# Kernel tuning notes

Hardware: AMD Instinct MI355X
Metric: run time of the kernel (lower is better)

The kernel has to match this reference:

```python
import jax, jax.numpy as jnp
import numpy as np
from jax import lax

B, T, D_IN, D_OUT = 1, 24000, 598, 3
UNITS = [100, 100, 100]
EPS = 0.001


def _lstm(x, W, U, b):
    # x: [B,T,D]; W: [D,4U]; U: [U,4U]; b: [4U]. Keras gate order i,f,g,o.
    units = U.shape[0]
    xW = jnp.einsum('btd,dk->btk', x, W) + b  # precompute input projections

    def step(carry, xw_t):
        h, c = carry
        z = xw_t + h @ U
        i, f, g, o = jnp.split(z, 4, axis=-1)
        c = jax.nn.sigmoid(f) * c + jax.nn.sigmoid(i) * jnp.tanh(g)
        h = jax.nn.sigmoid(o) * jnp.tanh(c)
        return (h, c), h

    h0 = jnp.zeros((x.shape[0], units), x.dtype)
    (_, _), hs = lax.scan(step, (h0, h0), jnp.swapaxes(xW, 0, 1))
    return jnp.swapaxes(hs, 0, 1)  # [B,T,U]


def _bn(x, gamma, beta, mean, var):
    # inference-mode batch norm over last axis
    return (x - mean) * lax.rsqrt(var + EPS) * gamma + beta


def setup_inputs() -> dict:
    key = jax.random.key(0)
    ks = jax.random.split(key, 16)
    out = {"x": jax.random.normal(ks[0], (B, T, D_IN), jnp.float32)}
    d_prev = D_IN
    ki = 1
    for l, u in enumerate(UNITS, start=1):
        out[f"W{l}"] = jax.random.normal(ks[ki], (d_prev, 4 * u), jnp.float32) * (2.0 / d_prev) ** 0.5; ki += 1
        out[f"U{l}"] = jax.random.normal(ks[ki], (u, 4 * u), jnp.float32) * (1.0 / u) ** 0.5; ki += 1
        out[f"b{l}"] = jnp.zeros((4 * u,), jnp.float32)
        out[f"g{l}"] = jnp.ones((u,), jnp.float32)
        out[f"be{l}"] = jnp.zeros((u,), jnp.float32)
        out[f"m{l}"] = jnp.zeros((u,), jnp.float32)
        out[f"v{l}"] = jnp.ones((u,), jnp.float32)
        d_prev = u
    out["Wd"] = jax.random.normal(ks[ki], (d_prev, D_OUT), jnp.float32) * (2.0 / d_prev) ** 0.5
    out["bd"] = jnp.zeros((D_OUT,), jnp.float32)
    return out


def reference(x, W1, U1, b1, g1, be1, m1, v1,
              W2, U2, b2, g2, be2, m2, v2,
              W3, U3, b3, g3, be3, m3, v3, Wd, bd):
    h = x
    params = [(W1, U1, b1, g1, be1, m1, v1),
              (W2, U2, b2, g2, be2, m2, v2),
              (W3, U3, b3, g3, be3, m3, v3)]
    for (W, U, b, g, be, m, v) in params:
        h = _lstm(h, W, U, b)
        h = _bn(h, g, be, m, v)
    return jax.nn.softmax(h @ Wd + bd, axis=-1)
```

## Files before the change

### kernel.cpp

```cpp
#include <hip/hip_runtime.h>

#define T_STEPS 24000
#define DIN 598
#define NU 100
#define NG 400
#define KHALF 52
#define KPAD 104
#define CHUNK 240
#define NCHUNK 100
#define RING 4
#define RN (RING * CHUNK)

#define BARRIER_LDS() asm volatile("s_waitcnt lgkmcnt(0)\n\ts_barrier" ::: "memory")

__device__ __forceinline__ void wg_wait_ge(int* flag, int target) {
    if (threadIdx.x == 0) {
        while (__hip_atomic_load(flag, __ATOMIC_RELAXED, __HIP_MEMORY_SCOPE_AGENT) < target)
            __builtin_amdgcn_s_sleep(2);
    }
    __syncthreads();
    __builtin_amdgcn_fence(__ATOMIC_ACQUIRE, "agent");
}
__device__ __forceinline__ void wg_publish(int* a, int va, int* b, int vb) {
    __syncthreads();
    if (threadIdx.x == 0) {
        if (a) __hip_atomic_store(a, va, __ATOMIC_RELEASE, __HIP_MEMORY_SCOPE_AGENT);
        if (b) __hip_atomic_store(b, vb, __ATOMIC_RELEASE, __HIP_MEMORY_SCOPE_AGENT);
    }
}

__device__ __forceinline__ float sigmoid_(float x) {
    return 1.f / (1.f + __expf(-x));
}
__device__ __forceinline__ float tanh_(float x) {
    float e = __expf(2.f * x);
    return 1.f - 2.f / (e + 1.f);
}

__global__ __launch_bounds__(256) void gemm_bias_kernel(
    const float* __restrict__ A, const float* __restrict__ B,
    const float* __restrict__ bias, float* __restrict__ C,
    int M, int N, int K)
{
    __shared__ float As[16][65];
    __shared__ float Bs[16][65];
    const int tid = threadIdx.x;
    const int tx = tid & 15;
    const int ty = tid >> 4;
    const int bm = blockIdx.y * 64;
    const int bn = blockIdx.x * 64;
    float acc[4][4] = {};

    for (int k0 = 0; k0 < K; k0 += 16) {
        #pragma unroll
        for (int p = 0; p < 4; ++p) {
            int e = tid + p * 256;
            int r = e >> 4, cc = e & 15;
            int m = bm + r, k = k0 + cc;
            float v = (m < M && k < K) ? A[(long)m * K + k] : 0.f;
            As[cc][r] = v;
        }
        #pragma unroll
        for (int p = 0; p < 4; ++p) {
            int e = tid + p * 256;
            int r = e >> 6, cc = e & 63;
            int k = k0 + r, n = bn + cc;
            float v = (k < K && n < N) ? B[(long)k * N + n] : 0.f;
            Bs[r][cc] = v;
        }
        __syncthreads();
        #pragma unroll
        for (int kk = 0; kk < 16; ++kk) {
            float a[4], b[4];
            #pragma unroll
            for (int i = 0; i < 4; ++i) a[i] = As[kk][ty * 4 + i];
            #pragma unroll
            for (int j = 0; j < 4; ++j) b[j] = Bs[kk][tx * 4 + j];
            #pragma unroll
            for (int i = 0; i < 4; ++i)
                #pragma unroll
                for (int j = 0; j < 4; ++j)
                    acc[i][j] += a[i] * b[j];
        }
        __syncthreads();
    }
    #pragma unroll
    for (int i = 0; i < 4; ++i) {
        int m = bm + ty * 4 + i;
        if (m >= M) continue;
        #pragma unroll
        for (int j = 0; j < 4; ++j) {
            int n = bn + tx * 4 + j;
            if (n < N) {
                int pn = (n % 100) * 4 + (n / 100);
                C[(long)m * N + pn] = acc[i][j] + bias[n];
            }
        }
    }
}

__device__ void rec_role(
    const float* __restrict__ xz, int xz_ring,
    const float* __restrict__ U,
    float* __restrict__ hout, long h_stride, int h_ring,
    int* flag_up, int* done_self, int* done_down, int* flag_self,
    float* lds)
{
    float* hb0 = lds;
    float* hb1 = lds + KPAD;
    const int tid = threadIdx.x;
    const bool active = tid < 2 * NU;
    const int u = tid >> 1;
    const int s = tid & 1;

    float4 uf[KHALF];
    if (active) {
        const int k0 = KHALF * s;
        #pragma unroll
        for (int i = 0; i < KHALF; ++i) {
            int k = k0 + i;
            uf[i] = (k < NU)
                ? make_float4(U[(long)k * NG + u],       U[(long)k * NG + NU + u],
                              U[(long)k * NG + 2 * NU + u], U[(long)k * NG + 3 * NU + u])
                : make_float4(0.f, 0.f, 0.f, 0.f);
        }
    }
    if (tid < KPAD) { hb0[tid] = 0.f; hb1[tid] = 0.f; }
    float c_state = 0.f;
    float2 xw0 = make_float2(0.f, 0.f), xw1 = xw0;
    float4 hbatch = make_float4(0.f, 0.f, 0.f, 0.f);
    __syncthreads();

    auto step = [&](const float* hrd, float* hwr, int t) {
        if (active) {
            const float4* h4 = (const float4*)(hrd + KHALF * s);
            float ax = 0.f, ay = 0.f, az = 0.f, aw = 0.f;
            #pragma unroll
            for (int q = 0; q < 13; ++q) {
                float4 hv = h4[q];
                float hh[4] = {hv.x, hv.y, hv.z, hv.w};
                #pragma unroll
                for (int j = 0; j < 4; ++j) {
                    float4 uv = uf[4 * q + j];
                    ax += uv.x * hh[j];
                    ay += uv.y * hh[j];
                    az += uv.z * hh[j];
                    aw += uv.w * hh[j];
                }
            }
            if (s == 0) { ax += xw0.x; ay += xw0.y; }
            else        { az += xw0.x; aw += xw0.y; }
            xw0 = xw1;
            int tp = t + 2;
            if (tp < T_STEPS) {
                long rr = xz_ring ? (long)(tp % RN) : (long)tp;
                xw1 = *(const float2*)&xz[rr * NG + 4 * u + 2 * s];
            }
            ax += __shfl_xor(ax, 1);
            ay += __shfl_xor(ay, 1);
            az += __shfl_xor(az, 1);
            aw += __shfl_xor(aw, 1);
            float iv = sigmoid_(ax);
            float fv = sigmoid_(ay);
            float gv = tanh_(az);
            float ov = sigmoid_(aw);
            c_state = fv * c_state + iv * gv;
            float h = ov * tanh_(c_state);
            if (s == 0) {
                hwr[u] = h;
                int ph = t & 3;
                if      (ph == 0) hbatch.x = h;
                else if (ph == 1) hbatch.y = h;
                else if (ph == 2) hbatch.z = h;
                else {
                    hbatch.w = h;
                    long tb = h_ring ? (long)((t - 3) % RN) : (long)(t - 3);
                    *(float4*)&hout[(long)u * h_stride + tb] = hbatch;
                }
            }
        }
        BARRIER_LDS();
    };

    for (int c = 0; c < NCHUNK; ++c) {
        if (flag_up) {
            int tgt = c + 2; if (tgt > NCHUNK) tgt = NCHUNK;
            wg_wait_ge(flag_up, tgt);
        }
        if (done_down && c >= RING) wg_wait_ge(done_down, c - RING + 1);
        if (c == 0 && active) {
            xw0 = *(const float2*)&xz[4 * u + 2 * s];
            xw1 = *(const float2*)&xz[NG + 4 * u + 2 * s];
        }
        const int t0 = c * CHUNK;
        for (int tt = 0; tt < CHUNK; tt += 2) {
            step(hb0, hb1, t0 + tt);
            step(hb1, hb0, t0 + tt + 1);
        }
        wg_publish(done_self, c + 1, flag_self, c + 1);
    }
}

__device__ void proj_role(
    const float* __restrict__ hin,
    const float* __restrict__ W,
    const float* __restrict__ bias,
    const float* __restrict__ g, const float* __restrict__ be,
    const float* __restrict__ m, const float* __restrict__ v,
    float* __restrict__ xzout,
    int* flag_up, int* done_self, int* done_down, int* flag_self,
    float* lds)
{
    const int tid = threadIdx.x;
    const bool active = tid < 2 * NU;
    const int u = tid >> 1;
    const int s = tid & 1;

    float4 wf[KHALF];
    float bx = 0.f, by = 0.f;
    if (active) {
        const int k0 = KHALF * s;
        float pbx = 0.f, pby = 0.f, pbz = 0.f, pbw = 0.f;
        #pragma unroll
        for (int i = 0; i < KHALF; ++i) {
            int k = k0 + i;
            if (k < NU) {
                float sc = g[k] * rsqrtf(v[k] + 1e-3f);
                float sh = be[k] - m[k] * sc;
                float w0 = W[(long)k * NG + u];
                float w1 = W[(long)k * NG + NU + u];
                float w2 = W[(long)k * NG + 2 * NU + u];
                float w3 = W[(long)k * NG + 3 * NU + u];
                wf[i] = make_float4(sc * w0, sc * w1, sc * w2, sc * w3);
                pbx += sh * w0; pby += sh * w1; pbz += sh * w2; pbw += sh * w3;
            } else {
                wf[i] = make_float4(0.f, 0.f, 0.f, 0.f);
            }
        }
        pbx += __shfl_xor(pbx, 1); pby += __shfl_xor(pby, 1);
        pbz += __shfl_xor(pbz, 1); pbw += __shfl_xor(pbw, 1);
        if (s == 0) { bx = bias[u]          + pbx; by = bias[NU + u]     + pby; }
        else        { bx = bias[2 * NU + u] + pbz; by = bias[3 * NU + u] + pbw; }
    }

    for (int c = 0; c < NCHUNK; ++c) {
        wg_wait_ge(flag_up, c + 1);
        if (c >= RING) wg_wait_ge(done_down, c - RING + 1);
        {
            const int tbase = (c % RING) * CHUNK;
            for (int idx = tid; idx < KPAD * CHUNK; idx += 256) {
                int k = idx / CHUNK, r = idx - k * CHUNK;
                lds[r * KPAD + k] = (k < NU) ? hin[(long)k * RN + tbase + r] : 0.f;
            }
        }
        wg_publish(done_self, c + 1, (int*)0, 0);
        if (active) {
            float* ob = xzout + (size_t)(c % RING) * CHUNK * NG;
            for (int r = 0; r < CHUNK; ++r) {
                const float4* h4 = (const float4*)(lds + r * KPAD + KHALF * s);
                float ax = 0.f, ay = 0.f, az = 0.f, aw = 0.f;
                #pragma unroll
                for (int q = 0; q < 13; ++q) {
                    float4 hv = h4[q];
                    float hh[4] = {hv.x, hv.y, hv.z, hv.w};
                    #pragma unroll
                    for (int j = 0; j < 4; ++j) {
                        float4 wv = wf[4 * q + j];
                        ax += wv.x * hh[j];
                        ay += wv.y * hh[j];
                        az += wv.z * hh[j];
                        aw += wv.w * hh[j];
                    }
                }
                ax += __shfl_xor(ax, 1);
                ay += __shfl_xor(ay, 1);
                az += __shfl_xor(az, 1);
                aw += __shfl_xor(aw, 1);
                float2 o2 = (s == 0) ? make_float2(ax + bx, ay + by)
                                     : make_float2(az + bx, aw + by);
                *(float2*)&ob[(long)r * NG + 4 * u + 2 * s] = o2;
            }
        }
        wg_publish(flag_self, c + 1, (int*)0, 0);
    }
}

__global__ __launch_bounds__(256, 1) void lstm_pipe_kernel(
    const float* xw1, const float* U1,
    const float* U2, const float* W2, const float* b2,
    const float* U3, const float* W3, const float* b3,
    const float* g1, const float* be1, const float* m1, const float* v1,
    const float* g2, const float* be2, const float* m2, const float* v2,
    float* h1r, float* h2r, float* xz2r, float* xz3r, float* h3,
    int* f)
{
    extern __shared__ float smem[];
    int* f_h1  = f +   0;
    int* d_p2  = f +  32;
    int* f_xz2 = f +  64;
    int* d_r2  = f +  96;
    int* f_h2  = f + 128;
    int* d_p3  = f + 160;
    int* f_xz3 = f + 192;
    int* d_r3  = f + 224;

    switch (blockIdx.x) {
    case 0: rec_role(xw1, 0, U1, h1r, RN, 1, (int*)0, (int*)0, d_p2, f_h1, smem); break;
    case 1: proj_role(h1r, W2, b2, g1, be1, m1, v1, xz2r, f_h1, d_p2, d_r2, f_xz2, smem); break;
    case 2: rec_role(xz2r, 1, U2, h2r, RN, 1, f_xz2, d_r2, d_p3, f_h2, smem); break;
    case 3: proj_role(h2r, W3, b3, g2, be2, m2, v2, xz3r, f_h2, d_p3, d_r3, f_xz3, smem); break;
    case 4: rec_role(xz3r, 1, U3, h3, T_STEPS, 0, f_xz3, d_r3, (int*)0, (int*)0, smem); break;
    }
}

__global__ __launch_bounds__(256) void dense_softmax_kernel(
    const float* __restrict__ H,
    const float* __restrict__ Wd,
    const float* __restrict__ bd,
    const float* __restrict__ g3, const float* __restrict__ be3,
    const float* __restrict__ m3, const float* __restrict__ v3,
    float* __restrict__ out, int T)
{
    __shared__ float w[300];
    __shared__ float b[3];
    const int tid = threadIdx.x;
    for (int i = tid; i < 300; i += 256) {
        int k = i / 3;
        float sc = g3[k] * rsqrtf(v3[k] + 1e-3f);
        w[i] = Wd[i] * sc;
    }
    if (tid < 3) {
        float acc = bd[tid];
        for (int k = 0; k < NU; ++k) {
            float sc = g3[k] * rsqrtf(v3[k] + 1e-3f);
            float sh = be3[k] - m3[k] * sc;
            acc += sh * Wd[3 * k + tid];
        }
        b[tid] = acc;
    }
    __syncthreads();

    int row = blockIdx.x * blockDim.x + tid;
    if (row >= T) return;
    float s0 = b[0], s1 = b[1], s2 = b[2];
    #pragma unroll 4
    for (int k = 0; k < NU; ++k) {
        float hv = H[(long)k * T + row];
        s0 += hv * w[3 * k + 0];
        s1 += hv * w[3 * k + 1];
        s2 += hv * w[3 * k + 2];
    }
    float mx = fmaxf(s0, fmaxf(s1, s2));
    float e0 = __expf(s0 - mx), e1 = __expf(s1 - mx), e2 = __expf(s2 - mx);
    float inv = 1.f / (e0 + e1 + e2);
    out[(long)row * 3 + 0] = e0 * inv;
    out[(long)row * 3 + 1] = e1 * inv;
    out[(long)row * 3 + 2] = e2 * inv;
}

extern "C" void kernel_launch(void* const* d_in, const int* in_sizes, int n_in,
                              void* d_out, int out_size, void* d_ws, size_t ws_size,
                              hipStream_t stream)
{
    const float* x   = (const float*)d_in[0];
    const float* W1  = (const float*)d_in[1];
    const float* U1  = (const float*)d_in[2];
    const float* b1  = (const float*)d_in[3];
    const float* ga1 = (const float*)d_in[4];
    const float* be1 = (const float*)d_in[5];
    const float* mu1 = (const float*)d_in[6];
    const float* va1 = (const float*)d_in[7];
    const float* W2  = (const float*)d_in[8];
    const float* U2  = (const float*)d_in[9];
    const float* b2  = (const float*)d_in[10];
    const float* ga2 = (const float*)d_in[11];
    const float* be2 = (const float*)d_in[12];
    const float* mu2 = (const float*)d_in[13];
    const float* va2 = (const float*)d_in[14];
    const float* W3  = (const float*)d_in[15];
    const float* U3  = (const float*)d_in[16];
    const float* b3  = (const float*)d_in[17];
    const float* ga3 = (const float*)d_in[18];
    const float* be3 = (const float*)d_in[19];
    const float* mu3 = (const float*)d_in[20];
    const float* va3 = (const float*)d_in[21];
    const float* Wd  = (const float*)d_in[22];
    const float* bd  = (const float*)d_in[23];

    float* xw1  = (float*)d_ws;
    float* h3   = xw1  + (size_t)T_STEPS * NG;
    float* h1r  = h3   + (size_t)T_STEPS * NU;
    float* h2r  = h1r  + (size_t)RN * NU;
    float* xz2r = h2r  + (size_t)RN * NU;
    float* xz3r = xz2r + (size_t)RN * NG;
    int*   flags = (int*)(xz3r + (size_t)RN * NG);
    float* out = (float*)d_out;

    dim3 blk(256);
    dim3 grd((NG + 63) / 64, (T_STEPS + 63) / 64);

    gemm_bias_kernel<<<grd, blk, 0, stream>>>(x, W1, b1, xw1, T_STEPS, NG, DIN);
    hipMemsetAsync(flags, 0, 512 * sizeof(int), stream);
    lstm_pipe_kernel<<<5, 256, CHUNK * KPAD * sizeof(float), stream>>>(
        xw1, U1, U2, W2, b2, U3, W3, b3,
        ga1, be1, mu1, va1, ga2, be2, mu2, va2,
        h1r, h2r, xz2r, xz3r, h3, flags);
    dense_softmax_kernel<<<(T_STEPS + 255) / 256, 256, 0, stream>>>(
        h3, Wd, bd, ga3, be3, mu3, va3, out, T_STEPS);
}
```

Baseline: 18.85 ms.

## Split LSTM recurrence gates across 4 lanes per unit with 512-thread blocks

```diff
diff --git a/kernel.cpp b/kernel.cpp
--- a/kernel.cpp
+++ b/kernel.cpp
@@ -10,6 +10,7 @@
 #define NCHUNK 100
 #define RING 4
 #define RN (RING * CHUNK)
+#define BLK 512
 
 #define BARRIER_LDS() asm volatile("s_waitcnt lgkmcnt(0)\n\ts_barrier" ::: "memory")
 
@@ -109,20 +110,21 @@
     float* hb0 = lds;
     float* hb1 = lds + KPAD;
     const int tid = threadIdx.x;
-    const bool active = tid < 2 * NU;
-    const int u = tid >> 1;
-    const int s = tid & 1;
-
-    float4 uf[KHALF];
+    const bool active = tid < 4 * NU;
+    const int u  = tid >> 2;
+    const int gp = (tid >> 1) & 1;
+    const int s  = tid & 1;
+
+    float2 uf[KHALF];
     if (active) {
         const int k0 = KHALF * s;
         #pragma unroll
         for (int i = 0; i < KHALF; ++i) {
             int k = k0 + i;
             uf[i] = (k < NU)
-                ? make_float4(U[(long)k * NG + u],       U[(long)k * NG + NU + u],
-                              U[(long)k * NG + 2 * NU + u], U[(long)k * NG + 3 * NU + u])
-                : make_float4(0.f, 0.f, 0.f, 0.f);
+                ? make_float2(U[(long)k * NG + 2 * gp * NU + u],
+                              U[(long)k * NG + (2 * gp + 1) * NU + u])
+                : make_float2(0.f, 0.f);
         }
     }
     if (tid < KPAD) { hb0[tid] = 0.f; hb1[tid] = 0.f; }
@@ -134,39 +136,40 @@
     auto step = [&](const float* hrd, float* hwr, int t) {
         if (active) {
             const float4* h4 = (const float4*)(hrd + KHALF * s);
-            float ax = 0.f, ay = 0.f, az = 0.f, aw = 0.f;
+            float ax = 0.f, ay = 0.f;
             #pragma unroll
             for (int q = 0; q < 13; ++q) {
                 float4 hv = h4[q];
                 float hh[4] = {hv.x, hv.y, hv.z, hv.w};
                 #pragma unroll
                 for (int j = 0; j < 4; ++j) {
-                    float4 uv = uf[4 * q + j];
+                    float2 uv = uf[4 * q + j];
                     ax += uv.x * hh[j];
                     ay += uv.y * hh[j];
-                    az += uv.z * hh[j];
-                    aw += uv.w * hh[j];
                 }
             }
-            if (s == 0) { ax += xw0.x; ay += xw0.y; }
-            else        { az += xw0.x; aw += xw0.y; }
+            if (s == gp) { ax += xw0.x; ay += xw0.y; }
             xw0 = xw1;
             int tp = t + 2;
             if (tp < T_STEPS) {
                 long rr = xz_ring ? (long)(tp % RN) : (long)tp;
-                xw1 = *(const float2*)&xz[rr * NG + 4 * u + 2 * s];
+                xw1 = *(const float2*)&xz[rr * NG + 4 * u + 2 * gp];
             }
             ax += __shfl_xor(ax, 1);
             ay += __shfl_xor(ay, 1);
-            az += __shfl_xor(az, 1);
-            aw += __shfl_xor(aw, 1);
-            float iv = sigmoid_(ax);
-            float fv = sigmoid_(ay);
-            float gv = tanh_(az);
-            float ov = sigmoid_(aw);
+            float bx = __shfl_xor(ax, 2);
+            float by = __shfl_xor(ay, 2);
+            float zi = gp ? bx : ax;
+            float zf = gp ? by : ay;
+            float zg = gp ? ax : bx;
+            float zo = gp ? ay : by;
+            float iv = sigmoid_(zi);
+            float fv = sigmoid_(zf);
+            float gv = tanh_(zg);
+            float ov = sigmoid_(zo);
             c_state = fv * c_state + iv * gv;
             float h = ov * tanh_(c_state);
-            if (s == 0) {
+            if ((tid & 3) == 0) {
                 hwr[u] = h;
                 int ph = t & 3;
                 if      (ph == 0) hbatch.x = h;
@@ -189,8 +192,8 @@
         }
         if (done_down && c >= RING) wg_wait_ge(done_down, c - RING + 1);
         if (c == 0 && active) {
-            xw0 = *(const float2*)&xz[4 * u + 2 * s];
-            xw1 = *(const float2*)&xz[NG + 4 * u + 2 * s];
+            xw0 = *(const float2*)&xz[4 * u + 2 * gp];
+            xw1 = *(const float2*)&xz[NG + 4 * u + 2 * gp];
         }
         const int t0 = c * CHUNK;
         for (int tt = 0; tt < CHUNK; tt += 2) {
@@ -212,35 +215,33 @@
     float* lds)
 {
     const int tid = threadIdx.x;
-    const bool active = tid < 2 * NU;
-    const int u = tid >> 1;
-    const int s = tid & 1;
-
-    float4 wf[KHALF];
+    const bool active = tid < 4 * NU;
+    const int u  = tid >> 2;
+    const int gp = (tid >> 1) & 1;
+    const int s  = tid & 1;
+
+    float2 wf[KHALF];
     float bx = 0.f, by = 0.f;
     if (active) {
         const int k0 = KHALF * s;
-        float pbx = 0.f, pby = 0.f, pbz = 0.f, pbw = 0.f;
+        float pbx = 0.f, pby = 0.f;
         #pragma unroll
         for (int i = 0; i < KHALF; ++i) {
             int k = k0 + i;
             if (k < NU) {
                 float sc = g[k] * rsqrtf(v[k] + 1e-3f);
                 float sh = be[k] - m[k] * sc;
-                float w0 = W[(long)k * NG + u];
-                float w1 = W[(long)k * NG + NU + u];
-                float w2 = W[(long)k * NG + 2 * NU + u];
-                float w3 = W[(long)k * NG + 3 * NU + u];
-                wf[i] = make_float4(sc * w0, sc * w1, sc * w2, sc * w3);
-                pbx += sh * w0; pby += sh * w1; pbz += sh * w2; pbw += sh * w3;
+                float w0 = W[(long)k * NG + 2 * gp * NU + u];
+                float w1 = W[(long)k * NG + (2 * gp + 1) * NU + u];
+                wf[i] = make_float2(sc * w0, sc * w1);
+                pbx += sh * w0; pby += sh * w1;
             } else {
-                wf[i] = make_float4(0.f, 0.f, 0.f, 0.f);
+                wf[i] = make_float2(0.f, 0.f);
             }
         }
         pbx += __shfl_xor(pbx, 1); pby += __shfl_xor(pby, 1);
-        pbz += __shfl_xor(pbz, 1); pbw += __shfl_xor(pbw, 1);
-        if (s == 0) { bx = bias[u]          + pbx; by = bias[NU + u]     + pby; }
-        else        { bx = bias[2 * NU + u] + pbz; by = bias[3 * NU + u] + pbw; }
+        bx = bias[2 * gp * NU + u]       + pbx;
+        by = bias[(2 * gp + 1) * NU + u] + pby;
     }
 
     for (int c = 0; c < NCHUNK; ++c) {
@@ -248,7 +249,7 @@
         if (c >= RING) wg_wait_ge(done_down, c - RING + 1);
         {
             const int tbase = (c % RING) * CHUNK;
-            for (int idx = tid; idx < KPAD * CHUNK; idx += 256) {
+            for (int idx = tid; idx < KPAD * CHUNK; idx += BLK) {
                 int k = idx / CHUNK, r = idx - k * CHUNK;
                 lds[r * KPAD + k] = (k < NU) ? hin[(long)k * RN + tbase + r] : 0.f;
             }
@@ -258,34 +259,30 @@
             float* ob = xzout + (size_t)(c % RING) * CHUNK * NG;
             for (int r = 0; r < CHUNK; ++r) {
                 const float4* h4 = (const float4*)(lds + r * KPAD + KHALF * s);
-                float ax = 0.f, ay = 0.f, az = 0.f, aw = 0.f;
+                float ax = 0.f, ay = 0.f;
                 #pragma unroll
                 for (int q = 0; q < 13; ++q) {
                     float4 hv = h4[q];
                     float hh[4] = {hv.x, hv.y, hv.z, hv.w};
                     #pragma unroll
                     for (int j = 0; j < 4; ++j) {
-                        float4 wv = wf[4 * q + j];
+                        float2 wv = wf[4 * q + j];
                         ax += wv.x * hh[j];
                         ay += wv.y * hh[j];
-                        az += wv.z * hh[j];
-                        aw += wv.w * hh[j];
                     }
                 }
                 ax += __shfl_xor(ax, 1);
                 ay += __shfl_xor(ay, 1);
-                az += __shfl_xor(az, 1);
-                aw += __shfl_xor(aw, 1);
-                float2 o2 = (s == 0) ? make_float2(ax + bx, ay + by)
-                                     : make_float2(az + bx, aw + by);
-                *(float2*)&ob[(long)r * NG + 4 * u + 2 * s] = o2;
+                if (s == 0)
+                    *(float2*)&ob[(long)r * NG + 4 * u + 2 * gp]
+                        = make_float2(ax + bx, ay + by);
             }
         }
         wg_publish(flag_self, c + 1, (int*)0, 0);
     }
 }
 
-__global__ __launch_bounds__(256, 1) void lstm_pipe_kernel(
+__global__ __launch_bounds__(BLK, 2) void lstm_pipe_kernel(
     const float* xw1, const float* U1,
     const float* U2, const float* W2, const float* b2,
     const float* U3, const float* W3, const float* b3,
@@ -401,7 +398,7 @@
 
     gemm_bias_kernel<<<grd, blk, 0, stream>>>(x, W1, b1, xw1, T_STEPS, NG, DIN);
     hipMemsetAsync(flags, 0, 512 * sizeof(int), stream);
-    lstm_pipe_kernel<<<5, 256, CHUNK * KPAD * sizeof(float), stream>>>(
+    lstm_pipe_kernel<<<5, BLK, CHUNK * KPAD * sizeof(float), stream>>>(
         xw1, U1, U2, W2, b2, U3, W3, b3,
         ga1, be1, mu1, va1, ga2, be2, mu2, va2,
         h1r, h2r, xz2r, xz3r, h3, flags);
```

New measurement: 21.57 ms. 1.14x slower.
